# Kernel optimization log

Measured on AMD Instinct MI355X. Metric: run time of the kernel, lower is better.

## Reference

```python
import jax, jax.numpy as jnp
import numpy as np

N = 100000      # nodes
E = 1600000     # edges
IN = 128        # in_dim
PE = 16         # pe_dim
HID = 128       # hid_dim
LAT = 64        # lat_dim
K = 4           # Chebyshev order


def setup_inputs() -> dict:
    key = jax.random.key(0)
    ks = jax.random.split(key, 12)
    f_in = IN + PE
    return {
        "x": jax.random.normal(ks[0], (N, IN), dtype=jnp.float32),
        "edge_index": jax.random.randint(ks[1], (2, E), 0, N, dtype=jnp.int32),
        "lap_pe": jax.random.normal(ks[2], (N, PE), dtype=jnp.float32),
        "edge_weight": jax.random.uniform(ks[3], (E,), dtype=jnp.float32),
        "W1": jax.random.normal(ks[4], (K, f_in, HID), dtype=jnp.float32) / np.sqrt(f_in),
        "b1": jnp.zeros((HID,), dtype=jnp.float32),
        "W2": jax.random.normal(ks[5], (K, HID, HID), dtype=jnp.float32) / np.sqrt(HID),
        "b2": jnp.zeros((HID,), dtype=jnp.float32),
        "W_mu": jax.random.normal(ks[6], (HID, LAT), dtype=jnp.float32) / np.sqrt(HID),
        "b_mu": jnp.zeros((LAT,), dtype=jnp.float32),
        "W_lv": jax.random.normal(ks[7], (HID, LAT), dtype=jnp.float32) / np.sqrt(HID),
        "b_lv": jnp.zeros((LAT,), dtype=jnp.float32),
    }


def _propagate(h, src, dst, w_hat):
    # (L_hat h)_i = sum_{(j->i)} w_hat_e * h_j   (one SpMM hop)
    return jax.ops.segment_sum(w_hat[:, None] * h[src], dst, num_segments=N)


def _cheb_conv(h, W, b, src, dst, w_hat):
    # PyG ChebConv recurrence: T0 = h, T1 = L_hat h, T_k = 2 L_hat T_{k-1} - T_{k-2}
    out = h @ W[0]
    tx0, tx1 = h, _propagate(h, src, dst, w_hat)
    out = out + tx1 @ W[1]
    for k in range(2, K):
        tx2 = 2.0 * _propagate(tx1, src, dst, w_hat) - tx0
        out = out + tx2 @ W[k]
        tx0, tx1 = tx1, tx2
    return out + b


def reference(x, edge_index, lap_pe, edge_weight, W1, b1, W2, b2, W_mu, b_mu, W_lv, b_lv):
    h = jnp.concatenate([x, lap_pe], axis=1)  # [N, IN+PE]
    src, dst = edge_index[0], edge_index[1]
    # ChebConv removes self loops before building the Laplacian -> zero their weight
    w = jnp.where(src == dst, 0.0, edge_weight)
    deg = jax.ops.segment_sum(w, src, num_segments=N)
    dinv = jnp.where(deg > 0, 1.0 / jnp.sqrt(deg), 0.0)
    # scaled Laplacian with lambda_max=2: L_hat = L - I = -D^{-1/2} A D^{-1/2}
    w_hat = -dinv[src] * w * dinv[dst]
    h = jax.nn.relu(_cheb_conv(h, W1, b1, src, dst, w_hat))
    h = jax.nn.relu(_cheb_conv(h, W2, b2, src, dst, w_hat))
    # scatter_mean with all-zero index == global mean pooling -> [1, HID]
    g = jnp.mean(h, axis=0, keepdims=True)
    return g @ W_mu + b_mu, g @ W_lv + b_lv
```

## Files before the change

kernel.cpp:

```cpp
#include <hip/hip_runtime.h>
#include <hip/hip_bf16.h>

#define IN_DIM 128
#define PE_DIM 16
#define F_IN 144
#define HID 128
#define LAT 64
#define K_CHEB 4

typedef unsigned int uint;
typedef unsigned short ushort;
typedef unsigned char uchar;
typedef __attribute__((ext_vector_type(8))) short short8;
typedef __attribute__((ext_vector_type(4))) float floatx4;
typedef __attribute__((ext_vector_type(2))) float floatx2;

__device__ __forceinline__ ushort f2bf(float f) {
    uint u = __float_as_uint(f);
    uint r = (u + 0x7FFFu + ((u >> 16) & 1u)) >> 16;
    return (ushort)r;
}
__device__ __forceinline__ uint bf_pack(float lo, float hi) {
    return (uint)f2bf(lo) | ((uint)f2bf(hi) << 16);
}

template<bool HI>
__device__ __forceinline__ floatx2 fp8x2_f32(uint v) {
    return __builtin_amdgcn_cvt_pk_f32_fp8((int)v, HI);
}
template<bool HI>
__device__ __forceinline__ uint f32_fp8x2(float a, float b, uint old) {
    return (uint)__builtin_amdgcn_cvt_pk_fp8_f32(a, b, (int)old, HI);
}

__global__ void zero_kernel(float* __restrict__ p, size_t n) {
    size_t i = (size_t)blockIdx.x * 256 + threadIdx.x;
    if (i < n) p[i] = 0.f;
}


__global__ __launch_bounds__(256) void bin_hist(const int* __restrict__ ei,
                                                int* __restrict__ ghA,
                                                int* __restrict__ ghB, int E) {
    __shared__ int hA[256], hB[256];
    int t = threadIdx.x;
    hA[t] = 0; hB[t] = 0;
    __syncthreads();
    int base = blockIdx.x * 4096;
#pragma unroll
    for (int j = 0; j < 16; j++) {
        int e = base + t + j * 256;
        if (e < E) {
            int s = ei[e], d = ei[E + e];
            atomicAdd(&hA[s >> 9], 1);
            atomicAdd(&hB[d >> 9], 1);
        }
    }
    __syncthreads();
    atomicAdd(&ghA[t], hA[t]);
    atomicAdd(&ghB[t], hB[t]);
}

__global__ __launch_bounds__(256) void bin_scan(const int* __restrict__ ghA,
                                                const int* __restrict__ ghB,
                                                int* __restrict__ bbA, int* __restrict__ curA,
                                                int* __restrict__ bbB, int* __restrict__ curB) {
    __shared__ int s[256];
    int t = threadIdx.x;
    int v = ghA[t];
    s[t] = v; __syncthreads();
    for (int off = 1; off < 256; off <<= 1) {
        int u = (t >= off) ? s[t - off] : 0;
        __syncthreads(); s[t] += u; __syncthreads();
    }
    bbA[t] = s[t] - v; curA[t] = s[t] - v;
    if (t == 255) bbA[256] = s[255];
    __syncthreads();
    int v2 = ghB[t];
    s[t] = v2; __syncthreads();
    for (int off = 1; off < 256; off <<= 1) {
        int u = (t >= off) ? s[t - off] : 0;
        __syncthreads(); s[t] += u; __syncthreads();
    }
    bbB[t] = s[t] - v2; curB[t] = s[t] - v2;
    if (t == 255) bbB[256] = s[255];
}

template<int BYDST>
__global__ __launch_bounds__(256) void bin_scatter(const int* __restrict__ ei,
                                                   const float* __restrict__ ew,
                                                   int* __restrict__ cursor,
                                                   uint2* __restrict__ outS, int E) {
    __shared__ uint2 rec[4096];
    __shared__ int pos[4096];
    __shared__ int hist[256], hscan[256], hrun[256], baseG[256];
    int t = threadIdx.x;
    hist[t] = 0;
    __syncthreads();
    int base = blockIdx.x * 4096;
    int cntBlk = E - base; if (cntBlk > 4096) cntBlk = 4096;
#pragma unroll
    for (int j = 0; j < 16; j++) {
        int e = base + t + j * 256;
        if (e < E) {
            int s = ei[e], d = ei[E + e];
            int key = BYDST ? d : s;
            atomicAdd(&hist[key >> 9], 1);
        }
    }
    __syncthreads();
    int v = hist[t];
    hscan[t] = v; __syncthreads();
    for (int off = 1; off < 256; off <<= 1) {
        int u = (t >= off) ? hscan[t - off] : 0;
        __syncthreads(); hscan[t] += u; __syncthreads();
    }
    int excl = hscan[t] - v;
    hscan[t] = excl;
    baseG[t] = atomicAdd(&cursor[t], v);
    hrun[t] = excl;
    __syncthreads();
#pragma unroll
    for (int j = 0; j < 16; j++) {
        int e = base + t + j * 256;
        if (e < E) {
            int s = ei[e], d = ei[E + e];
            float w = (s == d) ? 0.f : ew[e];
            int key = BYDST ? d : s;
            int b = key >> 9;
            int slot = atomicAdd(&hrun[b], 1);
            uint2 r;
            r.x = BYDST ? ((uint)s | ((uint)(d & 511) << 17)) : (uint)s;
            r.y = __float_as_uint(w);
            rec[slot] = r;
            pos[slot] = baseG[b] + (slot - hscan[b]);
        }
    }
    __syncthreads();
    for (int sI = t; sI < cntBlk; sI += 256) outS[pos[sI]] = rec[sI];
}

__global__ __launch_bounds__(256) void deg_bucket(const uint2* __restrict__ sA,
                                                  const int* __restrict__ bbA,
                                                  float* __restrict__ dinv, int N) {
    __shared__ float dl[512];
    int b = blockIdx.x, t = threadIdx.x;
    dl[t] = 0.f; dl[t + 256] = 0.f;
    __syncthreads();
    int s0 = bbA[b], s1 = bbA[b + 1];
    for (int r = s0 + t; r < s1; r += 256) {
        uint2 rc = sA[r];
        atomicAdd(&dl[(int)rc.x - (b << 9)], __uint_as_float(rc.y));
    }
    __syncthreads();
    for (int i = t; i < 512; i += 256) {
        int node = (b << 9) + i;
        if (node < N) {
            float d = dl[i];
            dinv[node] = (d > 0.f) ? rsqrtf(d) : 0.f;
        }
    }
}

__global__ __launch_bounds__(256) void csr_bucket(const uint2* __restrict__ sB,
                                                  const int* __restrict__ bbB,
                                                  const float* __restrict__ dinv,
                                                  int* __restrict__ rowp,
                                                  uint2* __restrict__ csr,
                                                  int N, int nbuck, int E) {
    __shared__ int cl[512], ol[512], orun[512];
    __shared__ float dvl[512];
    __shared__ int ps[256];
    int b = blockIdx.x, t = threadIdx.x;
    cl[t] = 0; cl[t + 256] = 0;
    for (int i = t; i < 512; i += 256) {
        int node = (b << 9) + i;
        dvl[i] = (node < N) ? dinv[node] : 0.f;
    }
    __syncthreads();
    int s0 = bbB[b], s1 = bbB[b + 1];
    for (int r = s0 + t; r < s1; r += 256)
        atomicAdd(&cl[(sB[r].x >> 17) & 511], 1);
    __syncthreads();
    int v0 = cl[2 * t], v1 = cl[2 * t + 1];
    int pv = v0 + v1;
    ps[t] = pv; __syncthreads();
    for (int off = 1; off < 256; off <<= 1) {
        int u = (t >= off) ? ps[t - off] : 0;
        __syncthreads(); ps[t] += u; __syncthreads();
    }
    int pexcl = ps[t] - pv;
    ol[2 * t] = pexcl;       ol[2 * t + 1] = pexcl + v0;
    orun[2 * t] = pexcl;     orun[2 * t + 1] = pexcl + v0;
    {
        int n0 = (b << 9) + 2 * t;
        if (n0 < N)     rowp[n0] = s0 + ol[2 * t];
        if (n0 + 1 < N) rowp[n0 + 1] = s0 + ol[2 * t + 1];
    }
    if (b == nbuck - 1 && t == 0) rowp[N] = E;
    __syncthreads();
    for (int r = s0 + t; r < s1; r += 256) {
        uint2 rc = sB[r];
        int src = rc.x & 0x1FFFF;
        int dl_ = (rc.x >> 17) & 511;
        float w = __uint_as_float(rc.y);
        int rank = atomicAdd(&orun[dl_], 1);
        float wh = -dinv[src] * w * dvl[dl_];
        uint2 o; o.x = (uint)src; o.y = __float_as_uint(wh);
        csr[s0 + rank] = o;
    }
}

__global__ void concat_x_fp8(const float* __restrict__ x, uint* __restrict__ T, size_t np) {
    size_t idx = (size_t)blockIdx.x * 256 + threadIdx.x;
    if (idx >= np) return;
    size_t i = idx >> 5; int p = (int)(idx & 31);
    float4 v = *(const float4*)(x + i * 128 + p * 4);
    uint o = f32_fp8x2<false>(v.x, v.y, 0u);
    o = f32_fp8x2<true>(v.z, v.w, o);
    T[i * 144 + p] = o;
}
__global__ void concat_pe_fp8(const float* __restrict__ pe, uint* __restrict__ T, size_t np) {
    size_t idx = (size_t)blockIdx.x * 256 + threadIdx.x;
    if (idx >= np) return;
    size_t i = idx >> 2; int p = (int)(idx & 3);
    float4 v = *(const float4*)(pe + i * 16 + p * 4);
    uint o = f32_fp8x2<false>(v.x, v.y, 0u);
    o = f32_fp8x2<true>(v.z, v.w, o);
    T[i * 144 + 32 + p] = o;
}

template<int K>
__global__ void wconv_kernel(const float* __restrict__ W, ushort* __restrict__ Bt) {
    int idx = blockIdx.x * 256 + threadIdx.x;
    if (idx >= 128 * K) return;
    int n = idx / K, kk = idx - n * K;
    Bt[idx] = f2bf(W[(size_t)kk * 128 + n]);
}

template<int F, int P>
__global__ __launch_bounds__(256) void prop_fp8(const uint* __restrict__ T,
                                                int off_src, int off_dst, int off_old,
                                                int recur,
                                                const int* __restrict__ rowp,
                                                const uint2* __restrict__ csrE, int n) {
    int node = blockIdx.x * 4 + (threadIdx.x >> 6);
    if (node >= n) return;
    int lane = threadIdx.x & 63;
    int g = lane >> 4;
    int ll = lane & 15;
    int e0 = rowp[node], e1 = rowp[node + 1];

    const uint* Tsrc = T + off_src;

    float acc[8];
#pragma unroll
    for (int i = 0; i < 8; i++) acc[i] = 0.f;
    float ex[4] = {0.f, 0.f, 0.f, 0.f};

    for (int base = e0; base < e1; base += 64) {
        int degc = e1 - base; if (degc > 64) degc = 64;
        int sidx = 0; float wval = 0.f;
        if (lane < degc) {
            uint2 rc = csrE[base + lane];
            sidx = (int)rc.x; wval = __uint_as_float(rc.y);
        }
        for (int j = 0; j < degc; j += 16) {
            int j0 = j + g, j1 = j0 + 4, j2 = j0 + 8, j3 = j0 + 12;
            int   s0 = __shfl(sidx, j0), s1 = __shfl(sidx, j1);
            int   s2 = __shfl(sidx, j2), s3 = __shfl(sidx, j3);
            float w0 = __shfl(wval, j0), w1 = __shfl(wval, j1);
            float w2 = __shfl(wval, j2), w3 = __shfl(wval, j3);
            const uint* hp0 = Tsrc + (size_t)s0 * P;
            const uint* hp1 = Tsrc + (size_t)s1 * P;
            const uint* hp2 = Tsrc + (size_t)s2 * P;
            const uint* hp3 = Tsrc + (size_t)s3 * P;
            uint2 v0 = *(const uint2*)(hp0 + ll * 2);
            uint2 v1 = *(const uint2*)(hp1 + ll * 2);
            uint2 v2 = *(const uint2*)(hp2 + ll * 2);
            uint2 v3 = *(const uint2*)(hp3 + ll * 2);
            uint x0 = 0, x1 = 0, x2 = 0, x3 = 0;
            if (F == 144) {
                if (ll < 4) {
                    x0 = hp0[32 + ll]; x1 = hp1[32 + ll];
                    x2 = hp2[32 + ll]; x3 = hp3[32 + ll];
                }
            }
#define ACC8(v, w) { \
            floatx2 f0 = fp8x2_f32<false>(v.x), f1 = fp8x2_f32<true>(v.x); \
            floatx2 f2 = fp8x2_f32<false>(v.y), f3 = fp8x2_f32<true>(v.y); \
            acc[0] += w * f0.x; acc[1] += w * f0.y; \
            acc[2] += w * f1.x; acc[3] += w * f1.y; \
            acc[4] += w * f2.x; acc[5] += w * f2.y; \
            acc[6] += w * f3.x; acc[7] += w * f3.y; }
            ACC8(v0, w0); ACC8(v1, w1); ACC8(v2, w2); ACC8(v3, w3);
#undef ACC8
            if (F == 144) {
                if (ll < 4) {
#define ACCX(xv, w) { \
                    floatx2 e0_ = fp8x2_f32<false>(xv), e1_ = fp8x2_f32<true>(xv); \
                    ex[0] += w * e0_.x; ex[1] += w * e0_.y; \
                    ex[2] += w * e1_.x; ex[3] += w * e1_.y; }
                    ACCX(x0, w0); ACCX(x1, w1); ACCX(x2, w2); ACCX(x3, w3);
#undef ACCX
                }
            }
        }
    }

#pragma unroll
    for (int i = 0; i < 8; i++) {
        acc[i] += __shfl_xor(acc[i], 16);
        acc[i] += __shfl_xor(acc[i], 32);
    }
    if (F == 144) {
#pragma unroll
        for (int i = 0; i < 4; i++) {
            ex[i] += __shfl_xor(ex[i], 16);
            ex[i] += __shfl_xor(ex[i], 32);
        }
    }

    if (g == 0) {
        uint* op = (uint*)T + off_dst + (size_t)node * P;
        const uint* tp = T + off_old + (size_t)node * P;
        if (recur) {
            uint2 ov = *(const uint2*)(tp + ll * 2);
            floatx2 f0 = fp8x2_f32<false>(ov.x), f1 = fp8x2_f32<true>(ov.x);
            floatx2 f2 = fp8x2_f32<false>(ov.y), f3 = fp8x2_f32<true>(ov.y);
            acc[0] = 2.f * acc[0] - f0.x; acc[1] = 2.f * acc[1] - f0.y;
            acc[2] = 2.f * acc[2] - f1.x; acc[3] = 2.f * acc[3] - f1.y;
            acc[4] = 2.f * acc[4] - f2.x; acc[5] = 2.f * acc[5] - f2.y;
            acc[6] = 2.f * acc[6] - f3.x; acc[7] = 2.f * acc[7] - f3.y;
            if (F == 144 && ll < 4) {
                uint ox = tp[32 + ll];
                floatx2 e0_ = fp8x2_f32<false>(ox), e1_ = fp8x2_f32<true>(ox);
                ex[0] = 2.f * ex[0] - e0_.x; ex[1] = 2.f * ex[1] - e0_.y;
                ex[2] = 2.f * ex[2] - e1_.x; ex[3] = 2.f * ex[3] - e1_.y;
            }
        }
        uint2 o;
        o.x = f32_fp8x2<false>(acc[0], acc[1], 0u);
        o.x = f32_fp8x2<true>(acc[2], acc[3], o.x);
        o.y = f32_fp8x2<false>(acc[4], acc[5], 0u);
        o.y = f32_fp8x2<true>(acc[6], acc[7], o.y);
        *(uint2*)(op + ll * 2) = o;
        if (F == 144 && ll < 4) {
            uint oe = f32_fp8x2<false>(ex[0], ex[1], 0u);
            oe = f32_fp8x2<true>(ex[2], ex[3], oe);
            op[32 + ll] = oe;
        }
    }
}

template<int K, bool REDUCE>
__global__ __launch_bounds__(256) void gemm_mfma(const uchar* __restrict__ A,
                                                 const ushort* __restrict__ Bt,
                                                 const float* __restrict__ bias,
                                                 uchar* __restrict__ Cb,
                                                 float* __restrict__ g,
                                                 int M, int CS) {
    __shared__ ushort As[128 * 40];
    __shared__ ushort Bs[128 * 40];
    __shared__ float colsum[128];
    int tid = threadIdx.x;
    int m0 = blockIdx.x * 128;
    int lane = tid & 63, wv = tid >> 6;
    int quad = lane >> 4, mrow = lane & 15;

    floatx4 acc[2][8];
#pragma unroll
    for (int mf = 0; mf < 2; mf++)
#pragma unroll
        for (int c = 0; c < 8; c++) acc[mf][c] = (floatx4){0.f, 0.f, 0.f, 0.f};
    if (REDUCE) { if (tid < 128) colsum[tid] = 0.f; }

    int ar = tid >> 1, ak = (tid & 1) * 16;
    int bn = tid >> 1, bk = (tid & 1) * 16;

    uint4 aReg = make_uint4(0u, 0u, 0u, 0u);
    if (m0 + ar < M) aReg = *(const uint4*)(A + (size_t)(m0 + ar) * K + ak);
    short8 bReg0 = *(const short8*)(Bt + (size_t)bn * K + bk);
    short8 bReg1 = *(const short8*)(Bt + (size_t)bn * K + bk + 8);

    for (int k0 = 0; k0 < K; k0 += 32) {
        floatx2 f0 = fp8x2_f32<false>(aReg.x), f1 = fp8x2_f32<true>(aReg.x);
        floatx2 f2 = fp8x2_f32<false>(aReg.y), f3 = fp8x2_f32<true>(aReg.y);
        floatx2 f4 = fp8x2_f32<false>(aReg.z), f5 = fp8x2_f32<true>(aReg.z);
        floatx2 f6 = fp8x2_f32<false>(aReg.w), f7 = fp8x2_f32<true>(aReg.w);
        uint4 p0, p1;
        p0.x = bf_pack(f0.x, f0.y); p0.y = bf_pack(f1.x, f1.y);
        p0.z = bf_pack(f2.x, f2.y); p0.w = bf_pack(f3.x, f3.y);
        p1.x = bf_pack(f4.x, f4.y); p1.y = bf_pack(f5.x, f5.y);
        p1.z = bf_pack(f6.x, f6.y); p1.w = bf_pack(f7.x, f7.y);
        *(uint4*)(&As[ar * 40 + ak]) = p0;
        *(uint4*)(&As[ar * 40 + ak + 8]) = p1;
        *(short8*)(&Bs[bn * 40 + bk]) = bReg0;
        *(short8*)(&Bs[bn * 40 + bk + 8]) = bReg1;
        __syncthreads();
        int kn = k0 + 32;
        if (kn < K) {
            aReg = make_uint4(0u, 0u, 0u, 0u);
            if (m0 + ar < M) aReg = *(const uint4*)(A + (size_t)(m0 + ar) * K + kn + ak);
            bReg0 = *(const short8*)(Bt + (size_t)bn * K + kn + bk);
            bReg1 = *(const short8*)(Bt + (size_t)bn * K + kn + bk + 8);
        }
        short8 af0 = *(const short8*)(&As[(wv * 32 + mrow) * 40 + quad * 8]);
        short8 af1 = *(const short8*)(&As[(wv * 32 + 16 + mrow) * 40 + quad * 8]);
#pragma unroll
        for (int c = 0; c < 8; c++) {
            short8 bf = *(const short8*)(&Bs[(c * 16 + mrow) * 40 + quad * 8]);
            acc[0][c] = __builtin_amdgcn_mfma_f32_16x16x32_bf16(af0, bf, acc[0][c], 0, 0, 0);
            acc[1][c] = __builtin_amdgcn_mfma_f32_16x16x32_bf16(af1, bf, acc[1][c], 0, 0, 0);
        }
        __syncthreads();
    }

#pragma unroll
    for (int c = 0; c < 8; c++) {
        int col = c * 16 + mrow;
        float bsv = bias[col];
        if (REDUCE) {
            float part = 0.f;
#pragma unroll
            for (int mf = 0; mf < 2; mf++)
#pragma unroll
                for (int r = 0; r < 4; r++) {
                    int row = m0 + wv * 32 + mf * 16 + quad * 4 + r;
                    if (row < M) {
                        float v = acc[mf][c][r] + bsv;
                        part += (v > 0.f) ? v : 0.f;
                    }
                }
            part += __shfl_xor(part, 16);
            part += __shfl_xor(part, 32);
            if (quad == 0) atomicAdd(&colsum[col], part);
        } else {
#pragma unroll
            for (int mf = 0; mf < 2; mf++)
#pragma unroll
                for (int r = 0; r < 4; r++) {
                    int row = m0 + wv * 32 + mf * 16 + quad * 4 + r;
                    if (row < M) {
                        float v = acc[mf][c][r] + bsv;
                        v = (v > 0.f) ? v : 0.f;
                        uint p = f32_fp8x2<false>(v, v, 0u);
                        Cb[(size_t)row * CS + col] = (uchar)(p & 0xFFu);
                    }
                }
        }
    }
    if (REDUCE) {
        __syncthreads();
        if (tid < 128) atomicAdd(&g[tid], colsum[tid]);
    }
}

__global__ void head_kernel(const float* __restrict__ g,
                            const float* __restrict__ Wmu, const float* __restrict__ bmu,
                            const float* __restrict__ Wlv, const float* __restrict__ blv,
                            float* __restrict__ out, float invN) {
    __shared__ float gm[128];
    int tid = threadIdx.x;
    gm[tid] = g[tid] * invN;
    __syncthreads();
    if (tid < 64) {
        float acc = bmu[tid];
        for (int i = 0; i < 128; i++) acc += gm[i] * Wmu[i * 64 + tid];
        out[tid] = acc;
    } else {
        int j = tid - 64;
        float acc = blv[j];
        for (int i = 0; i < 128; i++) acc += gm[i] * Wlv[i * 64 + j];
        out[64 + j] = acc;
    }
}

static inline size_t align64(size_t x) { return (x + 63) & ~(size_t)63; }

extern "C" void kernel_launch(void* const* d_in, const int* in_sizes, int n_in,
                              void* d_out, int out_size, void* d_ws, size_t ws_size,
                              hipStream_t stream) {
    const float* x   = (const float*)d_in[0];
    const int*   ei  = (const int*)d_in[1];
    const float* pe  = (const float*)d_in[2];
    const float* ew  = (const float*)d_in[3];
    const float* W1  = (const float*)d_in[4];
    const float* b1  = (const float*)d_in[5];
    const float* W2  = (const float*)d_in[6];
    const float* b2  = (const float*)d_in[7];
    const float* Wmu = (const float*)d_in[8];
    const float* bmu = (const float*)d_in[9];
    const float* Wlv = (const float*)d_in[10];
    const float* blv = (const float*)d_in[11];
    float* out = (float*)d_out;

    const int N = in_sizes[0] / IN_DIM;
    const int E = in_sizes[3];
    const int NBUCK = (N + 511) >> 9;
    const int NBLK  = (E + 4095) / 4096;

    float* ws = (float*)d_ws;
    size_t o_g    = 0;
    size_t o_ghA  = o_g + 128;
    size_t o_ghB  = o_ghA + 256;
    size_t zeroLen = o_ghB + 256;
    size_t o_bbA  = align64(zeroLen);
    size_t o_curA = align64(o_bbA + 257);
    size_t o_bbB  = align64(o_curA + 256);
    size_t o_curB = align64(o_bbB + 257);
    size_t o_rowp = align64(o_curB + 256);
    size_t o_dinv = align64(o_rowp + N + 1);
    size_t o_sA   = align64(o_dinv + N);
    size_t o_sB   = align64(o_sA + 2 * (size_t)E);
    size_t o_csr  = align64(o_sB + 2 * (size_t)E);
    size_t o_Bt1  = align64(o_csr + 2 * (size_t)E);
    size_t o_Bt2  = align64(o_Bt1 + 128 * 576 / 2);
    size_t o_T1   = align64(o_Bt2 + 128 * 512 / 2);
    size_t o_T2   = align64(o_T1 + (size_t)N * 144);

    float* g     = ws + o_g;
    int*   ghA   = (int*)(ws + o_ghA);
    int*   ghB   = (int*)(ws + o_ghB);
    int*   bbA   = (int*)(ws + o_bbA);
    int*   curA  = (int*)(ws + o_curA);
    int*   bbB   = (int*)(ws + o_bbB);
    int*   curB  = (int*)(ws + o_curB);
    int*   rowp  = (int*)(ws + o_rowp);
    float* dinv  = ws + o_dinv;
    uint2* sA    = (uint2*)(ws + o_sA);
    uint2* sB    = (uint2*)(ws + o_sB);
    uint2* csr   = (uint2*)(ws + o_csr);
    ushort* Bt1  = (ushort*)(ws + o_Bt1);
    ushort* Bt2  = (ushort*)(ws + o_Bt2);
    uint*  T1    = (uint*)(ws + o_T1);
    uint*  T2    = (uint*)(ws + o_T2);

    dim3 b256(256);

    zero_kernel<<<dim3((unsigned)((zeroLen + 255) / 256)), b256, 0, stream>>>(ws, zeroLen);
    bin_hist<<<dim3(NBLK), b256, 0, stream>>>(ei, ghA, ghB, E);
    bin_scan<<<dim3(1), b256, 0, stream>>>(ghA, ghB, bbA, curA, bbB, curB);
    bin_scatter<0><<<dim3(NBLK), b256, 0, stream>>>(ei, ew, curA, sA, E);
    deg_bucket<<<dim3(NBUCK), b256, 0, stream>>>(sA, bbA, dinv, N);
    bin_scatter<1><<<dim3(NBLK), b256, 0, stream>>>(ei, ew, curB, sB, E);
    csr_bucket<<<dim3(NBUCK), b256, 0, stream>>>(sB, bbB, dinv, rowp, csr, N, NBUCK, E);

    wconv_kernel<576><<<dim3((128 * 576 + 255) / 256), b256, 0, stream>>>(W1, Bt1);
    wconv_kernel<512><<<dim3((128 * 512 + 255) / 256), b256, 0, stream>>>(W2, Bt2);

    concat_x_fp8<<<dim3((unsigned)(((size_t)N * 32 + 255) / 256)), b256, 0, stream>>>(x, T1, (size_t)N * 32);
    concat_pe_fp8<<<dim3((unsigned)(((size_t)N * 4 + 255) / 256)), b256, 0, stream>>>(pe, T1, (size_t)N * 4);

    const unsigned propGrid = (unsigned)((N + 3) / 4);
    const unsigned gemmGrid = (unsigned)((N + 127) / 128);

    prop_fp8<144, 144><<<propGrid, b256, 0, stream>>>(T1, 0,  36,  0,  0, rowp, csr, N);
    prop_fp8<144, 144><<<propGrid, b256, 0, stream>>>(T1, 36, 72,  0,  1, rowp, csr, N);
    prop_fp8<144, 144><<<propGrid, b256, 0, stream>>>(T1, 72, 108, 36, 1, rowp, csr, N);
    gemm_mfma<576, false><<<gemmGrid, b256, 0, stream>>>((const uchar*)T1, Bt1, b1, (uchar*)T2, g, N, 512);

    prop_fp8<128, 128><<<propGrid, b256, 0, stream>>>(T2, 0,  32, 0,  0, rowp, csr, N);
    prop_fp8<128, 128><<<propGrid, b256, 0, stream>>>(T2, 32, 64, 0,  1, rowp, csr, N);
    prop_fp8<128, 128><<<propGrid, b256, 0, stream>>>(T2, 64, 96, 32, 1, rowp, csr, N);
    gemm_mfma<512, true><<<gemmGrid, b256, 0, stream>>>((const uchar*)T2, Bt2, b2, (uchar*)nullptr, g, N, 0);

    head_kernel<<<dim3(1), dim3(128), 0, stream>>>(g, Wmu, bmu, Wlv, blv, out, 1.0f / (float)N);
}
```

Baseline: 645.5 us.

## Fuse src/dst bin scatters into one pass and use nontemporal loads/stores

Merges the two bin_scatter launches (by source and by destination) into a single kernel that reads edge_index and edge weights once and writes both bucketed arrays. Block size drops to 2048 edges so the doubled shared-memory staging fits. Streaming accesses in deg_bucket, csr_bucket and the propagation kernel (CSR reads, recurrence operand reads, output writes) now use nontemporal loads and stores to reduce cache pollution. The risk is that nontemporal hints on data reused later, such as T buffers read by the next hop, could hurt L2 hit rates.

```diff
diff --git a/kernel.cpp b/kernel.cpp
--- a/kernel.cpp
+++ b/kernel.cpp
@@ -11,6 +11,7 @@
 typedef unsigned int uint;
 typedef unsigned short ushort;
 typedef unsigned char uchar;
+typedef unsigned long long ull;
 typedef __attribute__((ext_vector_type(8))) short short8;
 typedef __attribute__((ext_vector_type(4))) float floatx4;
 typedef __attribute__((ext_vector_type(2))) float floatx2;
@@ -31,6 +32,21 @@
 template<bool HI>
 __device__ __forceinline__ uint f32_fp8x2(float a, float b, uint old) {
     return (uint)__builtin_amdgcn_cvt_pk_fp8_f32(a, b, (int)old, HI);
+}
+
+__device__ __forceinline__ uint2 ntload_u2(const uint2* p) {
+    ull v = __builtin_nontemporal_load((const ull*)p);
+    uint2 r; r.x = (uint)v; r.y = (uint)(v >> 32); return r;
+}
+__device__ __forceinline__ void ntstore_u2(uint2* p, uint2 v) {
+    ull q = (ull)v.x | ((ull)v.y << 32);
+    __builtin_nontemporal_store(q, (ull*)p);
+}
+__device__ __forceinline__ uint ntload_u(const uint* p) {
+    return __builtin_nontemporal_load(p);
+}
+__device__ __forceinline__ void ntstore_u(uint* p, uint v) {
+    __builtin_nontemporal_store(v, p);
 }
 
 __global__ void zero_kernel(float* __restrict__ p, size_t n) {
@@ -86,58 +102,74 @@
     if (t == 255) bbB[256] = s[255];
 }
 
-template<int BYDST>
-__global__ __launch_bounds__(256) void bin_scatter(const int* __restrict__ ei,
-                                                   const float* __restrict__ ew,
-                                                   int* __restrict__ cursor,
-                                                   uint2* __restrict__ outS, int E) {
-    __shared__ uint2 rec[4096];
-    __shared__ int pos[4096];
-    __shared__ int hist[256], hscan[256], hrun[256], baseG[256];
+__global__ __launch_bounds__(256) void bin_scatter2(const int* __restrict__ ei,
+                                                    const float* __restrict__ ew,
+                                                    int* __restrict__ curA,
+                                                    int* __restrict__ curB,
+                                                    uint2* __restrict__ sA,
+                                                    uint2* __restrict__ sB, int E) {
+    __shared__ uint2 recA[2048]; __shared__ int posA[2048];
+    __shared__ uint2 recB[2048]; __shared__ int posB[2048];
+    __shared__ int hstA[256], scnA[256], runA[256], bgA[256];
+    __shared__ int hstB[256], scnB[256], runB[256], bgB[256];
     int t = threadIdx.x;
-    hist[t] = 0;
-    __syncthreads();
-    int base = blockIdx.x * 4096;
-    int cntBlk = E - base; if (cntBlk > 4096) cntBlk = 4096;
-#pragma unroll
-    for (int j = 0; j < 16; j++) {
+    hstA[t] = 0; hstB[t] = 0;
+    __syncthreads();
+    int base = blockIdx.x * 2048;
+    int cntBlk = E - base; if (cntBlk > 2048) cntBlk = 2048;
+    int sv[8], dv[8]; float wv[8];
+#pragma unroll
+    for (int j = 0; j < 8; j++) {
         int e = base + t + j * 256;
         if (e < E) {
-            int s = ei[e], d = ei[E + e];
-            int key = BYDST ? d : s;
-            atomicAdd(&hist[key >> 9], 1);
-        }
-    }
-    __syncthreads();
-    int v = hist[t];
-    hscan[t] = v; __syncthreads();
+            sv[j] = ei[e]; dv[j] = ei[E + e];
+            wv[j] = (sv[j] == dv[j]) ? 0.f : ew[e];
+            atomicAdd(&hstA[sv[j] >> 9], 1);
+            atomicAdd(&hstB[dv[j] >> 9], 1);
+        } else sv[j] = -1;
+    }
+    __syncthreads();
+    int vA = hstA[t];
+    scnA[t] = vA; __syncthreads();
     for (int off = 1; off < 256; off <<= 1) {
-        int u = (t >= off) ? hscan[t - off] : 0;
-        __syncthreads(); hscan[t] += u; __syncthreads();
-    }
-    int excl = hscan[t] - v;
-    hscan[t] = excl;
-    baseG[t] = atomicAdd(&cursor[t], v);
-    hrun[t] = excl;
-    __syncthreads();
-#pragma unroll
-    for (int j = 0; j < 16; j++) {
-        int e = base + t + j * 256;
-        if (e < E) {
-            int s = ei[e], d = ei[E + e];
-            float w = (s == d) ? 0.f : ew[e];
-            int key = BYDST ? d : s;
-            int b = key >> 9;
-            int slot = atomicAdd(&hrun[b], 1);
-            uint2 r;
-            r.x = BYDST ? ((uint)s | ((uint)(d & 511) << 17)) : (uint)s;
-            r.y = __float_as_uint(w);
-            rec[slot] = r;
-            pos[slot] = baseG[b] + (slot - hscan[b]);
-        }
-    }
-    __syncthreads();
-    for (int sI = t; sI < cntBlk; sI += 256) outS[pos[sI]] = rec[sI];
+        int u = (t >= off) ? scnA[t - off] : 0;
+        __syncthreads(); scnA[t] += u; __syncthreads();
+    }
+    int eA = scnA[t] - vA;
+    bgA[t] = atomicAdd(&curA[t], vA);
+    __syncthreads();
+    scnA[t] = eA; runA[t] = eA;
+    int vB = hstB[t];
+    scnB[t] = vB; __syncthreads();
+    for (int off = 1; off < 256; off <<= 1) {
+        int u = (t >= off) ? scnB[t - off] : 0;
+        __syncthreads(); scnB[t] += u; __syncthreads();
+    }
+    int eB = scnB[t] - vB;
+    bgB[t] = atomicAdd(&curB[t], vB);
+    __syncthreads();
+    scnB[t] = eB; runB[t] = eB;
+    __syncthreads();
+#pragma unroll
+    for (int j = 0; j < 8; j++) {
+        if (sv[j] >= 0) {
+            int bA = sv[j] >> 9;
+            int slot = atomicAdd(&runA[bA], 1);
+            uint2 r; r.x = (uint)sv[j]; r.y = __float_as_uint(wv[j]);
+            recA[slot] = r;
+            posA[slot] = bgA[bA] + (slot - scnA[bA]);
+            int bB = dv[j] >> 9;
+            int slot2 = atomicAdd(&runB[bB], 1);
+            uint2 r2; r2.x = (uint)sv[j] | ((uint)(dv[j] & 511) << 17); r2.y = __float_as_uint(wv[j]);
+            recB[slot2] = r2;
+            posB[slot2] = bgB[bB] + (slot2 - scnB[bB]);
+        }
+    }
+    __syncthreads();
+    for (int i = t; i < cntBlk; i += 256) {
+        ntstore_u2(&sA[posA[i]], recA[i]);
+        ntstore_u2(&sB[posB[i]], recB[i]);
+    }
 }
 
 __global__ __launch_bounds__(256) void deg_bucket(const uint2* __restrict__ sA,
@@ -149,7 +181,7 @@
     __syncthreads();
     int s0 = bbA[b], s1 = bbA[b + 1];
     for (int r = s0 + t; r < s1; r += 256) {
-        uint2 rc = sA[r];
+        uint2 rc = ntload_u2(&sA[r]);
         atomicAdd(&dl[(int)rc.x - (b << 9)], __uint_as_float(rc.y));
     }
     __syncthreads();
@@ -207,7 +239,7 @@
         int rank = atomicAdd(&orun[dl_], 1);
         float wh = -dinv[src] * w * dvl[dl_];
         uint2 o; o.x = (uint)src; o.y = __float_as_uint(wh);
-        csr[s0 + rank] = o;
+        ntstore_u2(&csr[s0 + rank], o);
     }
 }
 
@@ -262,7 +294,7 @@
         int degc = e1 - base; if (degc > 64) degc = 64;
         int sidx = 0; float wval = 0.f;
         if (lane < degc) {
-            uint2 rc = csrE[base + lane];
+            uint2 rc = ntload_u2(&csrE[base + lane]);
             sidx = (int)rc.x; wval = __uint_as_float(rc.y);
         }
         for (int j = 0; j < degc; j += 16) {
@@ -325,7 +357,7 @@
         uint* op = (uint*)T + off_dst + (size_t)node * P;
         const uint* tp = T + off_old + (size_t)node * P;
         if (recur) {
-            uint2 ov = *(const uint2*)(tp + ll * 2);
+            uint2 ov = ntload_u2((const uint2*)(tp + ll * 2));
             floatx2 f0 = fp8x2_f32<false>(ov.x), f1 = fp8x2_f32<true>(ov.x);
             floatx2 f2 = fp8x2_f32<false>(ov.y), f3 = fp8x2_f32<true>(ov.y);
             acc[0] = 2.f * acc[0] - f0.x; acc[1] = 2.f * acc[1] - f0.y;
@@ -333,7 +365,7 @@
             acc[4] = 2.f * acc[4] - f2.x; acc[5] = 2.f * acc[5] - f2.y;
             acc[6] = 2.f * acc[6] - f3.x; acc[7] = 2.f * acc[7] - f3.y;
             if (F == 144 && ll < 4) {
-                uint ox = tp[32 + ll];
+                uint ox = ntload_u(tp + 32 + ll);
                 floatx2 e0_ = fp8x2_f32<false>(ox), e1_ = fp8x2_f32<true>(ox);
                 ex[0] = 2.f * ex[0] - e0_.x; ex[1] = 2.f * ex[1] - e0_.y;
                 ex[2] = 2.f * ex[2] - e1_.x; ex[3] = 2.f * ex[3] - e1_.y;
@@ -344,11 +376,11 @@
         o.x = f32_fp8x2<true>(acc[2], acc[3], o.x);
         o.y = f32_fp8x2<false>(acc[4], acc[5], 0u);
         o.y = f32_fp8x2<true>(acc[6], acc[7], o.y);
-        *(uint2*)(op + ll * 2) = o;
+        ntstore_u2((uint2*)(op + ll * 2), o);
         if (F == 144 && ll < 4) {
             uint oe = f32_fp8x2<false>(ex[0], ex[1], 0u);
             oe = f32_fp8x2<true>(ex[2], ex[3], oe);
-            op[32 + ll] = oe;
+            ntstore_u(op + 32 + ll, oe);
         }
     }
 }
@@ -499,6 +531,7 @@
     const int E = in_sizes[3];
     const int NBUCK = (N + 511) >> 9;
     const int NBLK  = (E + 4095) / 4096;
+    const int NBLK2 = (E + 2047) / 2048;
 
     float* ws = (float*)d_ws;
     size_t o_g    = 0;
@@ -541,9 +574,8 @@
     zero_kernel<<<dim3((unsigned)((zeroLen + 255) / 256)), b256, 0, stream>>>(ws, zeroLen);
     bin_hist<<<dim3(NBLK), b256, 0, stream>>>(ei, ghA, ghB, E);
     bin_scan<<<dim3(1), b256, 0, stream>>>(ghA, ghB, bbA, curA, bbB, curB);
-    bin_scatter<0><<<dim3(NBLK), b256, 0, stream>>>(ei, ew, curA, sA, E);
+    bin_scatter2<<<dim3(NBLK2), b256, 0, stream>>>(ei, ew, curA, curB, sA, sB, E);
     deg_bucket<<<dim3(NBUCK), b256, 0, stream>>>(sA, bbA, dinv, N);
-    bin_scatter<1><<<dim3(NBLK), b256, 0, stream>>>(ei, ew, curB, sB, E);
     csr_bucket<<<dim3(NBUCK), b256, 0, stream>>>(sB, bbB, dinv, rowp, csr, N, NBUCK, E);
 
     wconv_kernel<576><<<dim3((128 * 576 + 255) / 256), b256, 0, stream>>>(W1, Bt1);
```

Result: slower. 692.9 us (+7.3%).
